# Optimization experiments

Measured on AMD Instinct MI355X. Metric: run time of the kernel, lower is better.

Reference implementation:

```python
import jax, jax.numpy as jnp
import numpy as np

DIM = 1024
NUM_HEADS = 16
HEAD_DIM = DIM // NUM_HEADS


def setup_inputs() -> dict:
    key = jax.random.key(0)
    k1, k2, k3 = jax.random.split(key, 3)
    x = jax.random.normal(k1, (2, 2048, DIM), dtype=jnp.float32)
    # nn.Linear weights stored as [out, in]; apply as x @ W.T
    w_qkv = jax.random.normal(k2, (3 * DIM, DIM), dtype=jnp.float32) * (1.0 / np.sqrt(DIM))
    w_out = jax.random.normal(k3, (DIM, DIM), dtype=jnp.float32) * (1.0 / np.sqrt(DIM))
    return {"x": x, "w_qkv": w_qkv, "w_out": w_out}


def reference(x, w_qkv, w_out):
    b, t, _ = x.shape
    qkv = x @ w_qkv.T                                  # [b, t, 3*dim]
    qkv = qkv.reshape(b, t, 3, NUM_HEADS, HEAD_DIM)    # (three h d) split order
    q, k, v = jnp.moveaxis(qkv, 2, 0)                  # each [b, t, h, d]
    q = q.transpose(0, 2, 1, 3)                        # [b, h, t, d]
    k = k.transpose(0, 2, 1, 3)
    v = v.transpose(0, 2, 1, 3)
    attn = jnp.einsum('bhid,bhjd->bhij', q, k) / np.sqrt(HEAD_DIM)
    causal_mask = jnp.triu(jnp.ones((t, t), dtype=bool), k=1)
    attn = jnp.where(causal_mask, -jnp.inf, attn)
    attn = jax.nn.softmax(attn, axis=-1)
    out = jnp.einsum('bhij,bhjd->bhid', attn, v)
    out = out.transpose(0, 2, 1, 3).reshape(b, t, DIM)
    return out @ w_out.T
```

## Files before the change

### kernel.cpp

```cpp
#include <hip/hip_runtime.h>

#define DIM_ 1024
#define HEADS_ 16
#define HD_ 64
#define T_ 2048
#define BATCH_ 2
#define QKVN_ 3072

typedef unsigned short u16;
typedef unsigned int u32;
typedef float f32x4 __attribute__((ext_vector_type(4)));
typedef float f32x16 __attribute__((ext_vector_type(16)));
typedef short s16x8 __attribute__((ext_vector_type(8)));
typedef unsigned short u16x4 __attribute__((ext_vector_type(4)));

__device__ __forceinline__ u16 f2bf(float f) {
  unsigned u = __float_as_uint(f);
  u += 0x7fffu + ((u >> 16) & 1u);
  return (u16)(u >> 16);
}

__device__ __forceinline__ float fexp2(float x) {
  float r;
  asm("v_exp_f32 %0, %1" : "=v"(r) : "v"(x));
  return r;
}

__device__ __forceinline__ float fmax3(float a, float b, float c) {
  float r;
  asm("v_max3_f32 %0, %1, %2, %3" : "=v"(r) : "v"(a), "v"(b), "v"(c));
  return r;
}

__device__ __forceinline__ u32 cvtpk(float a, float b) {
  u32 r;
  asm("v_cvt_pk_bf16_f32 %0, %1, %2" : "=v"(r) : "v"(a), "v"(b));
  return r;
}

__global__ __launch_bounds__(256) void cvt_all(const float* __restrict__ x,
                                               const float* __restrict__ wqkv,
                                               const float* __restrict__ wout,
                                               u16* __restrict__ outbase) {
  int i = blockIdx.x * 256 + threadIdx.x;
  const float4* src;
  int off;
  if (i < 1048576) { src = (const float4*)x; off = i; }
  else if (i < 1835008) { src = (const float4*)wqkv; off = i - 1048576; }
  else { src = (const float4*)wout; off = i - 1835008; }
  float4 v = src[off];
  u16x4 o;
  o.x = f2bf(v.x); o.y = f2bf(v.y); o.z = f2bf(v.z); o.w = f2bf(v.w);
  reinterpret_cast<u16x4*>(outbase)[i] = o;
}

__device__ __forceinline__ void gld_lds16(const void* g, void* l) {
  auto gp = (__attribute__((address_space(1))) char*)(unsigned long long)g;
  auto lp = (__attribute__((address_space(3))) char*)(unsigned int)(unsigned long long)l;
  __builtin_amdgcn_global_load_lds(gp, lp, 16, 0, 0);
}

template <int MODE>
__global__ __launch_bounds__(256) void gemm1(const u16* __restrict__ A,
                                             const u16* __restrict__ B,
                                             void* __restrict__ Cv,
                                             u16* __restrict__ vto) {
  constexpr int K = 1024;
  constexpr int NN = (MODE == 1) ? 1024 : QKVN_;
  constexpr int NT = (MODE == 1) ? 8 : 24;
  constexpr int CPX = (MODE == 1) ? 32 : 96;
  __shared__ __align__(16) u16 smem[32768];
  char* const smb = (char*)smem;
  const int bid = blockIdx.x;
  const int wk = (bid & 7) * CPX + (bid >> 3);
  const int mt = wk / NT, nt = wk % NT;
  const int tid = threadIdx.x;
  const int lane = tid & 63;
  const int w = tid >> 6;
  const int wr = w >> 1, wc = w & 1;
  const int lrow = lane & 15, kg = lane >> 4;
  const u16* Ag = A + (size_t)(mt * 128) * K;
  const u16* Bg = B + (size_t)(nt * 128) * K;

  f32x4 acc[4][4];
#pragma unroll
  for (int i = 0; i < 4; ++i)
#pragma unroll
    for (int j = 0; j < 4; ++j) {
      f32x4 z = {0.f, 0.f, 0.f, 0.f};
      acc[i][j] = z;
    }

  const int srow = tid >> 3;
  const int scol = 8 * ((tid & 7) ^ ((tid >> 3) & 7));
  const int ldsw = (tid & ~63) * 16;

  int aoff[4][2], boff[4][2];
#pragma unroll
  for (int mf = 0; mf < 4; ++mf)
#pragma unroll
    for (int ks = 0; ks < 2; ++ks) {
      aoff[mf][ks] = (wr * 64 + mf * 16 + lrow) * 128 + (((ks * 4 + kg) ^ (lrow & 7)) << 4);
      boff[mf][ks] = (wc * 64 + mf * 16 + lrow) * 128 + (((ks * 4 + kg) ^ (lrow & 7)) << 4);
    }

#pragma unroll
  for (int c = 0; c < 4; ++c) {
    gld_lds16(Ag + (size_t)(c * 32 + srow) * K + scol, smb + c * 4096 + ldsw);
    gld_lds16(Bg + (size_t)(c * 32 + srow) * K + scol, smb + 32768 + c * 4096 + ldsw);
  }

  int cur = 0;
  for (int k0 = 0; k0 < K; k0 += 64) {
    __syncthreads();
    if (k0 + 64 < K) {
      const int nb = (cur ^ 1) * 16384;
#pragma unroll
      for (int c = 0; c < 4; ++c) {
        gld_lds16(Ag + (size_t)(c * 32 + srow) * K + k0 + 64 + scol,
                  smb + nb + c * 4096 + ldsw);
        gld_lds16(Bg + (size_t)(c * 32 + srow) * K + k0 + 64 + scol,
                  smb + 32768 + nb + c * 4096 + ldsw);
      }
    }
    const char* Ac = smb + cur * 16384;
    const char* Bc = smb + 32768 + cur * 16384;
#pragma unroll
    for (int ks = 0; ks < 2; ++ks) {
      s16x8 a[4], b[4];
#pragma unroll
      for (int mf = 0; mf < 4; ++mf)
        a[mf] = *(const s16x8*)(Ac + aoff[mf][ks]);
#pragma unroll
      for (int nf = 0; nf < 4; ++nf)
        b[nf] = *(const s16x8*)(Bc + boff[nf][ks]);
#pragma unroll
      for (int mf = 0; mf < 4; ++mf)
#pragma unroll
        for (int nf = 0; nf < 4; ++nf)
          acc[mf][nf] = __builtin_amdgcn_mfma_f32_16x16x32_bf16(a[mf], b[nf], acc[mf][nf], 0, 0, 0);
    }
    cur ^= 1;
  }

  if (MODE == 1) {
    float* C = (float*)Cv;
#pragma unroll
    for (int mf = 0; mf < 4; ++mf)
#pragma unroll
      for (int nf = 0; nf < 4; ++nf)
#pragma unroll
        for (int j = 0; j < 4; ++j) {
          int r = mt * 128 + wr * 64 + mf * 16 + 4 * kg + j;
          int c = nt * 128 + wc * 64 + nf * 16 + lrow;
          C[(size_t)r * NN + c] = acc[mf][nf][j];
        }
  } else if (nt < 16) {
    u16* qkvo = (u16*)Cv;
#pragma unroll
    for (int mf = 0; mf < 4; ++mf)
#pragma unroll
      for (int nf = 0; nf < 4; ++nf)
#pragma unroll
        for (int j = 0; j < 4; ++j) {
          int r = mt * 128 + wr * 64 + mf * 16 + 4 * kg + j;
          int c = nt * 128 + wc * 64 + nf * 16 + lrow;
          qkvo[(size_t)r * QKVN_ + c] = f2bf(acc[mf][nf][j]);
        }
  } else {
    const int c16 = tid >> 4, chunk = tid & 15;
    const int bb = mt >> 4;
    const int tb = (mt & 15) * 128 + chunk * 8;
#pragma unroll
    for (int p = 0; p < 2; ++p) {
      __syncthreads();
      if (wc == p) {
#pragma unroll
        for (int mf = 0; mf < 4; ++mf)
#pragma unroll
          for (int nf = 0; nf < 4; ++nf) {
            const int cl = nf * 16 + lrow;
            const int rl = wr * 64 + mf * 16 + 4 * kg;
            u16x4 pk;
            pk.x = f2bf(acc[mf][nf][0]); pk.y = f2bf(acc[mf][nf][1]);
            pk.z = f2bf(acc[mf][nf][2]); pk.w = f2bf(acc[mf][nf][3]);
            *(u16x4*)&smem[cl * 136 + rl] = pk;
          }
      }
      __syncthreads();
#pragma unroll
      for (int pp = 0; pp < 4; ++pp) {
        const int cl = pp * 16 + c16;
        const int cg = nt * 128 + p * 64 + cl;
        const int hV = (cg >> 6) & 15, d = cg & 63;
        const s16x8 v = *(const s16x8*)&smem[cl * 136 + chunk * 8];
        *(s16x8*)(vto + ((size_t)((bb * 16 + hV) * 64 + d)) * T_ + tb) = v;
      }
    }
  }
}

__global__ __launch_bounds__(256, 2) void attn_fwd(const u16* __restrict__ qkv,
                                                   const u16* __restrict__ vt,
                                                   u16* __restrict__ o) {
  const int gid = blockIdx.x;
  const int gq = gid >> 3;
  const int bh = (gid & 7) * 4 + (gq >> 4);
  const int pr = gq & 15;
  const int b = bh >> 4, h = bh & 15;
  const int tid = threadIdx.x;
  const int lane = tid & 63;
  const int qw = (tid >> 6) & 1;
  const int kvg = tid >> 7;
  const int l31 = lane & 31, hi = lane >> 5;

  __shared__ __align__(16) char smem[65536];

  const int row_s = tid >> 3, slot_s = tid & 7;
  const u16* Kbase = qkv + (size_t)(b * T_) * QKVN_ + 1024 + h * 64;
  const u16* Vbase = vt + (size_t)(bh * 64) * T_;
  const u16* KgA = Kbase + (size_t)row_s * QKVN_ + slot_s * 8;
  const u16* KgB = KgA + (size_t)32 * QKVN_;
  const u16* VgA = Vbase + (size_t)row_s * T_ + slot_s * 8;
  const u16* VgB = VgA + (size_t)32 * T_;
  const int dstA = row_s * 128 + ((slot_s ^ (row_s & 7)) << 4);

  const int rbyte = l31 * 128;
  const int xsw = l31 & 7;
  const float CEXP = 0.18033688011112042f;

  for (int ph = 0; ph < 2; ++ph) {
    const int jt = (ph == 0) ? (31 - pr) : pr;
    const int nt = jt + 1;
    const int nrt = (nt + 1) >> 1;
    const int qrow0 = 64 * jt + 32 * qw;

    s16x8 qf[4];
    {
      const u16* qp = qkv + (size_t)(b * T_ + qrow0 + l31) * QKVN_ + h * 64 + 8 * hi;
#pragma unroll
      for (int ksl = 0; ksl < 4; ++ksl)
        qf[ksl] = *(const s16x8*)(qp + 16 * ksl);
    }

    f32x16 o0v, o1v;
#pragma unroll
    for (int r = 0; r < 16; ++r) { o0v[r] = 0.f; o1v[r] = 0.f; }
    float mrun = -__builtin_inff(), lrun = 0.0f;

    __syncthreads();
    *(s16x8*)(smem + dstA)                 = *(const s16x8*)KgA;
    *(s16x8*)(smem + 4096 + dstA)          = *(const s16x8*)KgB;
    *(s16x8*)(smem + 32768 + dstA)         = *(const s16x8*)VgA;
    *(s16x8*)(smem + 32768 + 4096 + dstA)  = *(const s16x8*)VgB;
    if (nt > 1) {
      *(s16x8*)(smem + 8192 + dstA)                = *(const s16x8*)(KgA + (size_t)64 * QKVN_);
      *(s16x8*)(smem + 8192 + 4096 + dstA)         = *(const s16x8*)(KgB + (size_t)64 * QKVN_);
      *(s16x8*)(smem + 32768 + 8192 + dstA)        = *(const s16x8*)(VgA + 64);
      *(s16x8*)(smem + 32768 + 8192 + 4096 + dstA) = *(const s16x8*)(VgB + 64);
    }

    int cur = 0;
    for (int r = 0; r < nrt; ++r) {
      const int t = 2 * r + kvg;
      const bool pe = (2 * r + 2 < nt), po = (2 * r + 3 < nt);
      s16x8 ke0, ke1, ve0, ve1, ko0, ko1, vo0, vo1;
      if (pe) {
        const size_t kofs = (size_t)(2 * r + 2) * 64 * QKVN_;
        const int vofs = (2 * r + 2) * 64;
        ke0 = *(const s16x8*)(KgA + kofs);
        ke1 = *(const s16x8*)(KgB + kofs);
        ve0 = *(const s16x8*)(VgA + vofs);
        ve1 = *(const s16x8*)(VgB + vofs);
      }
      if (po) {
        const size_t kofs = (size_t)(2 * r + 3) * 64 * QKVN_;
        const int vofs = (2 * r + 3) * 64;
        ko0 = *(const s16x8*)(KgA + kofs);
        ko1 = *(const s16x8*)(KgB + kofs);
        vo0 = *(const s16x8*)(VgA + vofs);
        vo1 = *(const s16x8*)(VgB + vofs);
      }
      __syncthreads();

      if (t < nt) {
        const char* Kc = smem + cur * 16384 + kvg * 8192;
        const char* Vc = smem + 32768 + cur * 16384 + kvg * 8192;
        const bool isdiag = (t == nt - 1);
        const bool two = !(isdiag && qw == 0);

        f32x16 s0v, s1v;
#pragma unroll
        for (int rr = 0; rr < 16; ++rr) { s0v[rr] = 0.f; s1v[rr] = 0.f; }
        __builtin_amdgcn_s_setprio(1);
#pragma unroll
        for (int ksl = 0; ksl < 4; ++ksl) {
          const s16x8 kf = *(const s16x8*)(Kc + rbyte + (((2 * ksl + hi) ^ xsw) << 4));
          s0v = __builtin_amdgcn_mfma_f32_32x32x16_bf16(kf, qf[ksl], s0v, 0, 0, 0);
        }
        if (two) {
#pragma unroll
          for (int ksl = 0; ksl < 4; ++ksl) {
            const s16x8 kf = *(const s16x8*)(Kc + 4096 + rbyte + (((2 * ksl + hi) ^ xsw) << 4));
            s1v = __builtin_amdgcn_mfma_f32_32x32x16_bf16(kf, qf[ksl], s1v, 0, 0, 0);
          }
        }
        __builtin_amdgcn_s_setprio(0);

        if (isdiag) {
          const int thr = 32 * qw + l31;
#pragma unroll
          for (int rr = 0; rr < 16; ++rr) {
            const int kvl = 4 * hi + (rr & 3) + 8 * (rr >> 2);
            if (kvl > thr) s0v[rr] = -__builtin_inff();
            if (two && kvl + 32 > thr) s1v[rr] = -__builtin_inff();
          }
        }

        float mloc = fmax3(s0v[0], s0v[1], s0v[2]);
#pragma unroll
        for (int rr = 3; rr < 15; rr += 2) mloc = fmax3(mloc, s0v[rr], s0v[rr + 1]);
        mloc = fmaxf(mloc, s0v[15]);
        if (two) {
          mloc = fmax3(mloc, s1v[0], s1v[1]);
#pragma unroll
          for (int rr = 2; rr < 16; rr += 2) mloc = fmax3(mloc, s1v[rr], s1v[rr + 1]);
        }
        mloc = fmaxf(mloc, __shfl_xor(mloc, 32));

        const bool needfull = !((mloc - mrun) * CEXP <= 8.0f);
        if (__any(needfull)) {
          const float newm = fmaxf(mrun, mloc);
          const float sc = fexp2((mrun - newm) * CEXP);
          mrun = newm;
          lrun *= sc;
          o0v *= sc;
          o1v *= sc;
        }
        const float msc = mrun * CEXP;

        float rs = 0.0f;
        u32 pd0[8], pd1[8];
#pragma unroll
        for (int ri = 0; ri < 8; ++ri) {
          const float p0 = fexp2(__builtin_fmaf(s0v[2 * ri], CEXP, -msc));
          const float p1 = fexp2(__builtin_fmaf(s0v[2 * ri + 1], CEXP, -msc));
          rs += p0 + p1;
          pd0[ri] = cvtpk(p0, p1);
        }
        if (two) {
#pragma unroll
          for (int ri = 0; ri < 8; ++ri) {
            const float p0 = fexp2(__builtin_fmaf(s1v[2 * ri], CEXP, -msc));
            const float p1 = fexp2(__builtin_fmaf(s1v[2 * ri + 1], CEXP, -msc));
            rs += p0 + p1;
            pd1[ri] = cvtpk(p0, p1);
          }
        }
        rs += __shfl_xor(rs, 32);
        lrun += rs;

        __builtin_amdgcn_s_setprio(1);
#pragma unroll
        for (int kk = 0; kk < 4; ++kk) {
          if (kk >= 2 && !two) break;
          u32 x0, y0, x1, y1;
          if (kk == 0)      { x0 = pd0[0]; y0 = pd0[2]; x1 = pd0[1]; y1 = pd0[3]; }
          else if (kk == 1) { x0 = pd0[4]; y0 = pd0[6]; x1 = pd0[5]; y1 = pd0[7]; }
          else if (kk == 2) { x0 = pd1[0]; y0 = pd1[2]; x1 = pd1[1]; y1 = pd1[3]; }
          else              { x0 = pd1[4]; y0 = pd1[6]; x1 = pd1[5]; y1 = pd1[7]; }
          asm volatile("v_permlane32_swap_b32 %0, %1" : "+v"(x0), "+v"(y0));
          asm volatile("v_permlane32_swap_b32 %0, %1" : "+v"(x1), "+v"(y1));
          u32 pw[4] = {x0, x1, y0, y1};
          const s16x8 pf = *(const s16x8*)pw;
          const s16x8 vf0 = *(const s16x8*)(Vc + rbyte + (((2 * kk + hi) ^ xsw) << 4));
          const s16x8 vf1 = *(const s16x8*)(Vc + 4096 + rbyte + (((2 * kk + hi) ^ xsw) << 4));
          o0v = __builtin_amdgcn_mfma_f32_32x32x16_bf16(vf0, pf, o0v, 0, 0, 0);
          o1v = __builtin_amdgcn_mfma_f32_32x32x16_bf16(vf1, pf, o1v, 0, 0, 0);
        }
        __builtin_amdgcn_s_setprio(0);
      }

      if (pe) {
        const int nb = (cur ^ 1) * 16384;
        *(s16x8*)(smem + nb + dstA)                = ke0;
        *(s16x8*)(smem + nb + 4096 + dstA)         = ke1;
        *(s16x8*)(smem + 32768 + nb + dstA)        = ve0;
        *(s16x8*)(smem + 32768 + nb + 4096 + dstA) = ve1;
      }
      if (po) {
        const int nb = (cur ^ 1) * 16384 + 8192;
        *(s16x8*)(smem + nb + dstA)                = ko0;
        *(s16x8*)(smem + nb + 4096 + dstA)         = ko1;
        *(s16x8*)(smem + 32768 + nb + dstA)        = vo0;
        *(s16x8*)(smem + 32768 + nb + 4096 + dstA) = vo1;
      }
      cur ^= 1;
    }

    __syncthreads();
    float* Om = (float*)smem + qw * 2048;
    float* Mf = (float*)(smem + 16384) + qw * 64;
    float* Lf = (float*)(smem + 16896) + qw * 64;
    if (kvg == 1) {
#pragma unroll
      for (int rr = 0; rr < 16; ++rr) {
        Om[rr * 64 + lane] = o0v[rr];
        Om[(16 + rr) * 64 + lane] = o1v[rr];
      }
      Mf[lane] = mrun;
      Lf[lane] = lrun;
    }
    __syncthreads();
    if (kvg == 0) {
      const float mA = Mf[lane];
      const float lA = Lf[lane];
      const float m2 = fmaxf(mrun, mA);
      const float sB = fexp2((mrun - m2) * CEXP);
      const float sA = fexp2((mA - m2) * CEXP);
      const float linv = 1.0f / (lrun * sB + lA * sA);
      u16* orow = o + (size_t)(b * T_ + qrow0 + l31) * DIM_ + h * 64;
#pragma unroll
      for (int ri = 0; ri < 8; ++ri) {
        const int dbase0 = 4 * hi + 8 * (ri >> 1) + 2 * (ri & 1);
        const float a0 = (o0v[2 * ri] * sB + Om[(2 * ri) * 64 + lane] * sA) * linv;
        const float a1 = (o0v[2 * ri + 1] * sB + Om[(2 * ri + 1) * 64 + lane] * sA) * linv;
        const float c0 = (o1v[2 * ri] * sB + Om[(16 + 2 * ri) * 64 + lane] * sA) * linv;
        const float c1 = (o1v[2 * ri + 1] * sB + Om[(16 + 2 * ri + 1) * 64 + lane] * sA) * linv;
        *(u32*)(orow + dbase0) = cvtpk(a0, a1);
        *(u32*)(orow + 32 + dbase0) = cvtpk(c0, c1);
      }
    }
  }
}

extern "C" void kernel_launch(void* const* d_in, const int* in_sizes, int n_in,
                              void* d_out, int out_size, void* d_ws, size_t ws_size,
                              hipStream_t stream) {
  const float* x = (const float*)d_in[0];
  const float* w_qkv = (const float*)d_in[1];
  const float* w_out = (const float*)d_in[2];
  char* ws = (char*)d_ws;
  u16* xb    = (u16*)(ws + 0);
  u16* wqkvb = (u16*)(ws + 8388608);
  u16* woutb = (u16*)(ws + 14680064);
  u16* qkvb  = (u16*)(ws + 16777216);
  u16* vtb   = (u16*)(ws + 41943040);
  u16* attno = (u16*)(ws + 50331648);

  cvt_all<<<8192, 256, 0, stream>>>(x, w_qkv, w_out, xb);
  gemm1<2><<<768, 256, 0, stream>>>(xb, wqkvb, qkvb, vtb);
  attn_fwd<<<512, 256, 0, stream>>>(qkvb, vtb, attno);
  gemm1<1><<<256, 256, 0, stream>>>(attno, woutb, d_out, nullptr);
}
```

Measured before the change: 90.34 us.

## Process both paired query tiles concurrently in 512-thread blocks sharing K/V loads

The attention kernel used to handle its two causal-paired query tiles (31-pr and pr) one after the other in a 256-thread block. It now launches 512 threads so both tiles run at the same time in separate wave groups. Each K/V tile is loaded into shared memory once per block and reused by both query halves, and the load work is spread over twice as many threads. In exchange, the waves on the short tile sit idle at barriers while the long tile finishes. Larger blocks may also lower occupancy, since the launch bound changed from (256,2) to 512.

```diff
diff --git a/kernel.cpp b/kernel.cpp
--- a/kernel.cpp
+++ b/kernel.cpp
@@ -200,9 +200,9 @@
   }
 }
 
-__global__ __launch_bounds__(256, 2) void attn_fwd(const u16* __restrict__ qkv,
-                                                   const u16* __restrict__ vt,
-                                                   u16* __restrict__ o) {
+__global__ __launch_bounds__(512) void attn_fwd(const u16* __restrict__ qkv,
+                                                const u16* __restrict__ vt,
+                                                u16* __restrict__ o) {
   const int gid = blockIdx.x;
   const int gq = gid >> 3;
   const int bh = (gid & 7) * 4 + (gq >> 4);
@@ -210,226 +210,207 @@
   const int b = bh >> 4, h = bh & 15;
   const int tid = threadIdx.x;
   const int lane = tid & 63;
-  const int qw = (tid >> 6) & 1;
-  const int kvg = tid >> 7;
+  const int w8 = tid >> 6;
+  const int qhalf = w8 >> 2;
+  const int qw = (w8 >> 1) & 1;
+  const int kvg = w8 & 1;
   const int l31 = lane & 31, hi = lane >> 5;
+
+  const int jt = qhalf ? pr : (31 - pr);
+  const int nt = jt + 1;
+  const int ntmax = 32 - pr;
+  const int nrt = (ntmax + 1) >> 1;
+  const int qrow0 = 64 * jt + 32 * qw;
 
   __shared__ __align__(16) char smem[65536];
 
   const int row_s = tid >> 3, slot_s = tid & 7;
   const u16* Kbase = qkv + (size_t)(b * T_) * QKVN_ + 1024 + h * 64;
   const u16* Vbase = vt + (size_t)(bh * 64) * T_;
-  const u16* KgA = Kbase + (size_t)row_s * QKVN_ + slot_s * 8;
-  const u16* KgB = KgA + (size_t)32 * QKVN_;
-  const u16* VgA = Vbase + (size_t)row_s * T_ + slot_s * 8;
-  const u16* VgB = VgA + (size_t)32 * T_;
-  const int dstA = row_s * 128 + ((slot_s ^ (row_s & 7)) << 4);
+  const u16* Kg = Kbase + (size_t)row_s * QKVN_ + slot_s * 8;
+  const u16* Vg = Vbase + (size_t)row_s * T_ + slot_s * 8;
+  const int dst = row_s * 128 + ((slot_s ^ (row_s & 7)) << 4);
 
   const int rbyte = l31 * 128;
   const int xsw = l31 & 7;
   const float CEXP = 0.18033688011112042f;
 
-  for (int ph = 0; ph < 2; ++ph) {
-    const int jt = (ph == 0) ? (31 - pr) : pr;
-    const int nt = jt + 1;
-    const int nrt = (nt + 1) >> 1;
-    const int qrow0 = 64 * jt + 32 * qw;
-
-    s16x8 qf[4];
-    {
-      const u16* qp = qkv + (size_t)(b * T_ + qrow0 + l31) * QKVN_ + h * 64 + 8 * hi;
-#pragma unroll
-      for (int ksl = 0; ksl < 4; ++ksl)
-        qf[ksl] = *(const s16x8*)(qp + 16 * ksl);
-    }
-
-    f32x16 o0v, o1v;
-#pragma unroll
-    for (int r = 0; r < 16; ++r) { o0v[r] = 0.f; o1v[r] = 0.f; }
-    float mrun = -__builtin_inff(), lrun = 0.0f;
-
+  s16x8 qf[4];
+  {
+    const u16* qp = qkv + (size_t)(b * T_ + qrow0 + l31) * QKVN_ + h * 64 + 8 * hi;
+#pragma unroll
+    for (int ksl = 0; ksl < 4; ++ksl)
+      qf[ksl] = *(const s16x8*)(qp + 16 * ksl);
+  }
+
+  f32x16 o0v, o1v;
+#pragma unroll
+  for (int r = 0; r < 16; ++r) { o0v[r] = 0.f; o1v[r] = 0.f; }
+  float mrun = -__builtin_inff(), lrun = 0.0f;
+
+  *(s16x8*)(smem + dst)                 = *(const s16x8*)Kg;
+  *(s16x8*)(smem + 32768 + dst)         = *(const s16x8*)Vg;
+  *(s16x8*)(smem + 8192 + dst)          = *(const s16x8*)(Kg + (size_t)64 * QKVN_);
+  *(s16x8*)(smem + 32768 + 8192 + dst)  = *(const s16x8*)(Vg + 64);
+
+  int cur = 0;
+  for (int r = 0; r < nrt; ++r) {
+    const int t = 2 * r + kvg;
+    const bool pe = (2 * r + 2 < ntmax), po = (2 * r + 3 < ntmax);
+    s16x8 ke, ve, ko, vo;
+    if (pe) {
+      ke = *(const s16x8*)(Kg + (size_t)(2 * r + 2) * 64 * QKVN_);
+      ve = *(const s16x8*)(Vg + (2 * r + 2) * 64);
+    }
+    if (po) {
+      ko = *(const s16x8*)(Kg + (size_t)(2 * r + 3) * 64 * QKVN_);
+      vo = *(const s16x8*)(Vg + (2 * r + 3) * 64);
+    }
     __syncthreads();
-    *(s16x8*)(smem + dstA)                 = *(const s16x8*)KgA;
-    *(s16x8*)(smem + 4096 + dstA)          = *(const s16x8*)KgB;
-    *(s16x8*)(smem + 32768 + dstA)         = *(const s16x8*)VgA;
-    *(s16x8*)(smem + 32768 + 4096 + dstA)  = *(const s16x8*)VgB;
-    if (nt > 1) {
-      *(s16x8*)(smem + 8192 + dstA)                = *(const s16x8*)(KgA + (size_t)64 * QKVN_);
-      *(s16x8*)(smem + 8192 + 4096 + dstA)         = *(const s16x8*)(KgB + (size_t)64 * QKVN_);
-      *(s16x8*)(smem + 32768 + 8192 + dstA)        = *(const s16x8*)(VgA + 64);
-      *(s16x8*)(smem + 32768 + 8192 + 4096 + dstA) = *(const s16x8*)(VgB + 64);
-    }
-
-    int cur = 0;
-    for (int r = 0; r < nrt; ++r) {
-      const int t = 2 * r + kvg;
-      const bool pe = (2 * r + 2 < nt), po = (2 * r + 3 < nt);
-      s16x8 ke0, ke1, ve0, ve1, ko0, ko1, vo0, vo1;
-      if (pe) {
-        const size_t kofs = (size_t)(2 * r + 2) * 64 * QKVN_;
-        const int vofs = (2 * r + 2) * 64;
-        ke0 = *(const s16x8*)(KgA + kofs);
-        ke1 = *(const s16x8*)(KgB + kofs);
-        ve0 = *(const s16x8*)(VgA + vofs);
-        ve1 = *(const s16x8*)(VgB + vofs);
-      }
-      if (po) {
-        const size_t kofs = (size_t)(2 * r + 3) * 64 * QKVN_;
-        const int vofs = (2 * r + 3) * 64;
-        ko0 = *(const s16x8*)(KgA + kofs);
-        ko1 = *(const s16x8*)(KgB + kofs);
-        vo0 = *(const s16x8*)(VgA + vofs);
-        vo1 = *(const s16x8*)(VgB + vofs);
-      }
-      __syncthreads();
-
-      if (t < nt) {
-        const char* Kc = smem + cur * 16384 + kvg * 8192;
-        const char* Vc = smem + 32768 + cur * 16384 + kvg * 8192;
-        const bool isdiag = (t == nt - 1);
-        const bool two = !(isdiag && qw == 0);
-
-        f32x16 s0v, s1v;
-#pragma unroll
-        for (int rr = 0; rr < 16; ++rr) { s0v[rr] = 0.f; s1v[rr] = 0.f; }
-        __builtin_amdgcn_s_setprio(1);
+
+    if (t < nt) {
+      const char* Kc = smem + cur * 16384 + kvg * 8192;
+      const char* Vc = smem + 32768 + cur * 16384 + kvg * 8192;
+      const bool isdiag = (t == nt - 1);
+      const bool two = !(isdiag && qw == 0);
+
+      f32x16 s0v, s1v;
+#pragma unroll
+      for (int rr = 0; rr < 16; ++rr) { s0v[rr] = 0.f; s1v[rr] = 0.f; }
+      __builtin_amdgcn_s_setprio(1);
+#pragma unroll
+      for (int ksl = 0; ksl < 4; ++ksl) {
+        const s16x8 kf = *(const s16x8*)(Kc + rbyte + (((2 * ksl + hi) ^ xsw) << 4));
+        s0v = __builtin_amdgcn_mfma_f32_32x32x16_bf16(kf, qf[ksl], s0v, 0, 0, 0);
+      }
+      if (two) {
 #pragma unroll
         for (int ksl = 0; ksl < 4; ++ksl) {
-          const s16x8 kf = *(const s16x8*)(Kc + rbyte + (((2 * ksl + hi) ^ xsw) << 4));
-          s0v = __builtin_amdgcn_mfma_f32_32x32x16_bf16(kf, qf[ksl], s0v, 0, 0, 0);
+          const s16x8 kf = *(const s16x8*)(Kc + 4096 + rbyte + (((2 * ksl + hi) ^ xsw) << 4));
+          s1v = __builtin_amdgcn_mfma_f32_32x32x16_bf16(kf, qf[ksl], s1v, 0, 0, 0);
         }
-        if (two) {
-#pragma unroll
-          for (int ksl = 0; ksl < 4; ++ksl) {
-            const s16x8 kf = *(const s16x8*)(Kc + 4096 + rbyte + (((2 * ksl + hi) ^ xsw) << 4));
-            s1v = __builtin_amdgcn_mfma_f32_32x32x16_bf16(kf, qf[ksl], s1v, 0, 0, 0);
-          }
+      }
+      __builtin_amdgcn_s_setprio(0);
+
+      if (isdiag) {
+        const int thr = 32 * qw + l31;
+#pragma unroll
+        for (int rr = 0; rr < 16; ++rr) {
+          const int kvl = 4 * hi + (rr & 3) + 8 * (rr >> 2);
+          if (kvl > thr) s0v[rr] = -__builtin_inff();
+          if (two && kvl + 32 > thr) s1v[rr] = -__builtin_inff();
         }
-        __builtin_amdgcn_s_setprio(0);
-
-        if (isdiag) {
-          const int thr = 32 * qw + l31;
-#pragma unroll
-          for (int rr = 0; rr < 16; ++rr) {
-            const int kvl = 4 * hi + (rr & 3) + 8 * (rr >> 2);
-            if (kvl > thr) s0v[rr] = -__builtin_inff();
-            if (two && kvl + 32 > thr) s1v[rr] = -__builtin_inff();
-          }
+      }
+
+      float mloc = fmax3(s0v[0], s0v[1], s0v[2]);
+#pragma unroll
+      for (int rr = 3; rr < 15; rr += 2) mloc = fmax3(mloc, s0v[rr], s0v[rr + 1]);
+      mloc = fmaxf(mloc, s0v[15]);
+      if (two) {
+        mloc = fmax3(mloc, s1v[0], s1v[1]);
+#pragma unroll
+        for (int rr = 2; rr < 16; rr += 2) mloc = fmax3(mloc, s1v[rr], s1v[rr + 1]);
+      }
+      mloc = fmaxf(mloc, __shfl_xor(mloc, 32));
+
+      const bool needfull = !((mloc - mrun) * CEXP <= 8.0f);
+      if (__any(needfull)) {
+        const float newm = fmaxf(mrun, mloc);
+        const float sc = fexp2((mrun - newm) * CEXP);
+        mrun = newm;
+        lrun *= sc;
+        o0v *= sc;
+        o1v *= sc;
+      }
+      const float msc = mrun * CEXP;
+
+      float rs = 0.0f;
+      u32 pd0[8], pd1[8];
+#pragma unroll
+      for (int ri = 0; ri < 8; ++ri) {
+        const float p0 = fexp2(__builtin_fmaf(s0v[2 * ri], CEXP, -msc));
+        const float p1 = fexp2(__builtin_fmaf(s0v[2 * ri + 1], CEXP, -msc));
+        rs += p0 + p1;
+        pd0[ri] = cvtpk(p0, p1);
+      }
+      if (two) {
+#pragma unroll
+        for (int ri = 0; ri < 8; ++ri) {
+          const float p0 = fexp2(__builtin_fmaf(s1v[2 * ri], CEXP, -msc));
+          const float p1 = fexp2(__builtin_fmaf(s1v[2 * ri + 1], CEXP, -msc));
+          rs += p0 + p1;
+          pd1[ri] = cvtpk(p0, p1);
         }
-
-        float mloc = fmax3(s0v[0], s0v[1], s0v[2]);
-#pragma unroll
-        for (int rr = 3; rr < 15; rr += 2) mloc = fmax3(mloc, s0v[rr], s0v[rr + 1]);
-        mloc = fmaxf(mloc, s0v[15]);
-        if (two) {
-          mloc = fmax3(mloc, s1v[0], s1v[1]);
-#pragma unroll
-          for (int rr = 2; rr < 16; rr += 2) mloc = fmax3(mloc, s1v[rr], s1v[rr + 1]);
-        }
-        mloc = fmaxf(mloc, __shfl_xor(mloc, 32));
-
-        const bool needfull = !((mloc - mrun) * CEXP <= 8.0f);
-        if (__any(needfull)) {
-          const float newm = fmaxf(mrun, mloc);
-          const float sc = fexp2((mrun - newm) * CEXP);
-          mrun = newm;
-          lrun *= sc;
-          o0v *= sc;
-          o1v *= sc;
-        }
-        const float msc = mrun * CEXP;
-
-        float rs = 0.0f;
-        u32 pd0[8], pd1[8];
-#pragma unroll
-        for (int ri = 0; ri < 8; ++ri) {
-          const float p0 = fexp2(__builtin_fmaf(s0v[2 * ri], CEXP, -msc));
-          const float p1 = fexp2(__builtin_fmaf(s0v[2 * ri + 1], CEXP, -msc));
-          rs += p0 + p1;
-          pd0[ri] = cvtpk(p0, p1);
-        }
-        if (two) {
-#pragma unroll
-          for (int ri = 0; ri < 8; ++ri) {
-            const float p0 = fexp2(__builtin_fmaf(s1v[2 * ri], CEXP, -msc));
-            const float p1 = fexp2(__builtin_fmaf(s1v[2 * ri + 1], CEXP, -msc));
-            rs += p0 + p1;
-            pd1[ri] = cvtpk(p0, p1);
-          }
-        }
-        rs += __shfl_xor(rs, 32);
-        lrun += rs;
-
-        __builtin_amdgcn_s_setprio(1);
-#pragma unroll
-        for (int kk = 0; kk < 4; ++kk) {
-          if (kk >= 2 && !two) break;
-          u32 x0, y0, x1, y1;
-          if (kk == 0)      { x0 = pd0[0]; y0 = pd0[2]; x1 = pd0[1]; y1 = pd0[3]; }
-          else if (kk == 1) { x0 = pd0[4]; y0 = pd0[6]; x1 = pd0[5]; y1 = pd0[7]; }
-          else if (kk == 2) { x0 = pd1[0]; y0 = pd1[2]; x1 = pd1[1]; y1 = pd1[3]; }
-          else              { x0 = pd1[4]; y0 = pd1[6]; x1 = pd1[5]; y1 = pd1[7]; }
-          asm volatile("v_permlane32_swap_b32 %0, %1" : "+v"(x0), "+v"(y0));
-          asm volatile("v_permlane32_swap_b32 %0, %1" : "+v"(x1), "+v"(y1));
-          u32 pw[4] = {x0, x1, y0, y1};
-          const s16x8 pf = *(const s16x8*)pw;
-          const s16x8 vf0 = *(const s16x8*)(Vc + rbyte + (((2 * kk + hi) ^ xsw) << 4));
-          const s16x8 vf1 = *(const s16x8*)(Vc + 4096 + rbyte + (((2 * kk + hi) ^ xsw) << 4));
-          o0v = __builtin_amdgcn_mfma_f32_32x32x16_bf16(vf0, pf, o0v, 0, 0, 0);
-          o1v = __builtin_amdgcn_mfma_f32_32x32x16_bf16(vf1, pf, o1v, 0, 0, 0);
-        }
-        __builtin_amdgcn_s_setprio(0);
-      }
-
-      if (pe) {
-        const int nb = (cur ^ 1) * 16384;
-        *(s16x8*)(smem + nb + dstA)                = ke0;
-        *(s16x8*)(smem + nb + 4096 + dstA)         = ke1;
-        *(s16x8*)(smem + 32768 + nb + dstA)        = ve0;
-        *(s16x8*)(smem + 32768 + nb + 4096 + dstA) = ve1;
-      }
-      if (po) {
-        const int nb = (cur ^ 1) * 16384 + 8192;
-        *(s16x8*)(smem + nb + dstA)                = ko0;
-        *(s16x8*)(smem + nb + 4096 + dstA)         = ko1;
-        *(s16x8*)(smem + 32768 + nb + dstA)        = vo0;
-        *(s16x8*)(smem + 32768 + nb + 4096 + dstA) = vo1;
-      }
-      cur ^= 1;
-    }
-
-    __syncthreads();
-    float* Om = (float*)smem + qw * 2048;
-    float* Mf = (float*)(smem + 16384) + qw * 64;
-    float* Lf = (float*)(smem + 16896) + qw * 64;
-    if (kvg == 1) {
-#pragma unroll
-      for (int rr = 0; rr < 16; ++rr) {
-        Om[rr * 64 + lane] = o0v[rr];
-        Om[(16 + rr) * 64 + lane] = o1v[rr];
-      }
-      Mf[lane] = mrun;
-      Lf[lane] = lrun;
-    }
-    __syncthreads();
-    if (kvg == 0) {
-      const float mA = Mf[lane];
-      const float lA = Lf[lane];
-      const float m2 = fmaxf(mrun, mA);
-      const float sB = fexp2((mrun - m2) * CEXP);
-      const float sA = fexp2((mA - m2) * CEXP);
-      const float linv = 1.0f / (lrun * sB + lA * sA);
-      u16* orow = o + (size_t)(b * T_ + qrow0 + l31) * DIM_ + h * 64;
-#pragma unroll
-      for (int ri = 0; ri < 8; ++ri) {
-        const int dbase0 = 4 * hi + 8 * (ri >> 1) + 2 * (ri & 1);
-        const float a0 = (o0v[2 * ri] * sB + Om[(2 * ri) * 64 + lane] * sA) * linv;
-        const float a1 = (o0v[2 * ri + 1] * sB + Om[(2 * ri + 1) * 64 + lane] * sA) * linv;
-        const float c0 = (o1v[2 * ri] * sB + Om[(16 + 2 * ri) * 64 + lane] * sA) * linv;
-        const float c1 = (o1v[2 * ri + 1] * sB + Om[(16 + 2 * ri + 1) * 64 + lane] * sA) * linv;
-        *(u32*)(orow + dbase0) = cvtpk(a0, a1);
-        *(u32*)(orow + 32 + dbase0) = cvtpk(c0, c1);
-      }
+      }
+      rs += __shfl_xor(rs, 32);
+      lrun += rs;
+
+      __builtin_amdgcn_s_setprio(1);
+#pragma unroll
+      for (int kk = 0; kk < 4; ++kk) {
+        if (kk >= 2 && !two) break;
+        u32 x0, y0, x1, y1;
+        if (kk == 0)      { x0 = pd0[0]; y0 = pd0[2]; x1 = pd0[1]; y1 = pd0[3]; }
+        else if (kk == 1) { x0 = pd0[4]; y0 = pd0[6]; x1 = pd0[5]; y1 = pd0[7]; }
+        else if (kk == 2) { x0 = pd1[0]; y0 = pd1[2]; x1 = pd1[1]; y1 = pd1[3]; }
+        else              { x0 = pd1[4]; y0 = pd1[6]; x1 = pd1[5]; y1 = pd1[7]; }
+        asm volatile("v_permlane32_swap_b32 %0, %1" : "+v"(x0), "+v"(y0));
+        asm volatile("v_permlane32_swap_b32 %0, %1" : "+v"(x1), "+v"(y1));
+        u32 pw[4] = {x0, x1, y0, y1};
+        const s16x8 pf = *(const s16x8*)pw;
+        const s16x8 vf0 = *(const s16x8*)(Vc + rbyte + (((2 * kk + hi) ^ xsw) << 4));
+        const s16x8 vf1 = *(const s16x8*)(Vc + 4096 + rbyte + (((2 * kk + hi) ^ xsw) << 4));
+        o0v = __builtin_amdgcn_mfma_f32_32x32x16_bf16(vf0, pf, o0v, 0, 0, 0);
+        o1v = __builtin_amdgcn_mfma_f32_32x32x16_bf16(vf1, pf, o1v, 0, 0, 0);
+      }
+      __builtin_amdgcn_s_setprio(0);
+    }
+
+    if (pe) {
+      const int nb = (cur ^ 1) * 16384;
+      *(s16x8*)(smem + nb + dst)         = ke;
+      *(s16x8*)(smem + 32768 + nb + dst) = ve;
+    }
+    if (po) {
+      const int nb = (cur ^ 1) * 16384 + 8192;
+      *(s16x8*)(smem + nb + dst)         = ko;
+      *(s16x8*)(smem + 32768 + nb + dst) = vo;
+    }
+    cur ^= 1;
+  }
+
+  __syncthreads();
+  const int qidx = qhalf * 2 + qw;
+  float* Om = (float*)smem + qidx * 2048;
+  float* Mf = (float*)(smem + 32768) + qidx * 64;
+  float* Lf = (float*)(smem + 33792) + qidx * 64;
+  if (kvg == 1) {
+#pragma unroll
+    for (int rr = 0; rr < 16; ++rr) {
+      Om[rr * 64 + lane] = o0v[rr];
+      Om[(16 + rr) * 64 + lane] = o1v[rr];
+    }
+    Mf[lane] = mrun;
+    Lf[lane] = lrun;
+  }
+  __syncthreads();
+  if (kvg == 0) {
+    const float mA = Mf[lane];
+    const float lA = Lf[lane];
+    const float m2 = fmaxf(mrun, mA);
+    const float sB = fexp2((mrun - m2) * CEXP);
+    const float sA = fexp2((mA - m2) * CEXP);
+    const float linv = 1.0f / (lrun * sB + lA * sA);
+    u16* orow = o + (size_t)(b * T_ + qrow0 + l31) * DIM_ + h * 64;
+#pragma unroll
+    for (int ri = 0; ri < 8; ++ri) {
+      const int dbase0 = 4 * hi + 8 * (ri >> 1) + 2 * (ri & 1);
+      const float a0 = (o0v[2 * ri] * sB + Om[(2 * ri) * 64 + lane] * sA) * linv;
+      const float a1 = (o0v[2 * ri + 1] * sB + Om[(2 * ri + 1) * 64 + lane] * sA) * linv;
+      const float c0 = (o1v[2 * ri] * sB + Om[(16 + 2 * ri) * 64 + lane] * sA) * linv;
+      const float c1 = (o1v[2 * ri + 1] * sB + Om[(16 + 2 * ri + 1) * 64 + lane] * sA) * linv;
+      *(u32*)(orow + dbase0) = cvtpk(a0, a1);
+      *(u32*)(orow + 32 + dbase0) = cvtpk(c0, c1);
     }
   }
 }
@@ -450,6 +431,6 @@
 
   cvt_all<<<8192, 256, 0, stream>>>(x, w_qkv, w_out, xb);
   gemm1<2><<<768, 256, 0, stream>>>(xb, wqkvb, qkvb, vtb);
-  attn_fwd<<<512, 256, 0, stream>>>(qkvb, vtb, attno);
+  attn_fwd<<<512, 512, 0, stream>>>(qkvb, vtb, attno);
   gemm1<1><<<256, 256, 0, stream>>>(attno, woutb, d_out, nullptr);
 }
```

Result: slower. 101.7 us (+12.6%).
